# Performance work log

Hardware: AMD Instinct MI355X
Metric: run time of the kernel (lower is better)

Reference implementation:

```python
import jax, jax.numpy as jnp
import numpy as np

SLIDING_WINDOW = 512
LOGIT_SOFTCAP = 50.0
NEG_INF = -1e30


def setup_inputs() -> dict:
    key = jax.random.key(0)
    ks = jax.random.split(key, 3)
    B, S, H, KVH, D, BS = 4, 1024, 32, 8, 128, 64
    nb = S // BS          # blocks per sequence = 16
    nblocks = B * nb      # total cache blocks = 64
    total = B * S         # flattened tokens = 4096
    return {
        "query": jax.random.normal(ks[0], (total, H, D), dtype=jnp.float32),
        "key": jax.random.normal(ks[1], (total, KVH, D), dtype=jnp.float32),
        "value": jax.random.normal(ks[2], (total, KVH, D), dtype=jnp.float32),
        "k_cache": jnp.zeros((nblocks, BS, KVH, D), dtype=jnp.float32),
        "v_cache": jnp.zeros((nblocks, BS, KVH, D), dtype=jnp.float32),
        "block_offsets": jnp.arange(nblocks, dtype=jnp.int32).reshape(B, nb),
    }


def reference(query, key, value, k_cache, v_cache, block_offsets):
    B, nb = block_offsets.shape
    nblocks, BS, KVH, D = k_cache.shape
    S = nb * BS
    H = query.shape[1]
    G = H // KVH  # GQA group size
    scale = D ** -0.5

    flat_blocks = block_offsets.reshape(-1)  # [B*nb]
    # 1) write new keys/values into the paged cache per the block table
    k_cache = k_cache.at[flat_blocks].set(key.reshape(-1, BS, KVH, D))
    v_cache = v_cache.at[flat_blocks].set(value.reshape(-1, BS, KVH, D))
    # 2) gather per-sequence contiguous K/V from cache blocks
    k = k_cache[flat_blocks].reshape(B, S, KVH, D)
    v = v_cache[flat_blocks].reshape(B, S, KVH, D)

    q = query.reshape(B, S, KVH, G, D)
    scores = jnp.einsum("bqhgd,bkhd->bhgqk", q, k) * scale
    # logit softcapping (Gemma-style)
    scores = jnp.tanh(scores / LOGIT_SOFTCAP) * LOGIT_SOFTCAP
    # causal + sliding-window mask
    i = jnp.arange(S)[:, None]
    j = jnp.arange(S)[None, :]
    mask = (j <= i) & ((i - j) < SLIDING_WINDOW)
    scores = jnp.where(mask, scores, NEG_INF)
    p = jax.nn.softmax(scores, axis=-1)
    out = jnp.einsum("bhgqk,bkhd->bqhgd", p, v)
    return out.reshape(B * S, H, D)
```

## Files before the change

### kernel.cpp

```cpp
#include <hip/hip_runtime.h>
#include <hip/hip_bf16.h>

typedef __bf16 bf16_t;
typedef bf16_t bf16x8 __attribute__((ext_vector_type(8)));
typedef bf16_t bf16x4 __attribute__((ext_vector_type(4)));
typedef bf16_t bf16x2 __attribute__((ext_vector_type(2)));
typedef float f32x4 __attribute__((ext_vector_type(4)));

#define B_   4
#define S_   1024
#define H_   32
#define KVH_ 8
#define D_   128
#define WIN_ 512
#define KVD_ (KVH_ * D_)
#define LOG2E_ 1.4426950408889634f
#define C1_ (2.0f * (0.08838834764831845f / 50.0f) * LOG2E_)
#define K2_ (50.0f * LOG2E_)
#define NK22_ (-2.0f * K2_)
#define EXP2F_(x) __builtin_amdgcn_exp2f(x)

__global__ __launch_bounds__(512, 4) void attn_fwd(
    const float* __restrict__ Q, const float* __restrict__ K,
    const float* __restrict__ V, float* __restrict__ Out)
{
  const int fid = blockIdx.x + 32 * (blockIdx.y + 8 * (int)blockIdx.z);
  const int swz = (fid & 7) * 128 + (fid >> 3);
  const int i0  = (swz & 31) * 32;
  const int kvh = (swz >> 5) & 7;
  const int b   = swz >> 8;

  const int tid  = threadIdx.x;
  const int w    = tid >> 6;
  const int lane = tid & 63;
  const int m16  = lane & 15;
  const int quad = lane >> 4;
  const int g    = w & 3;
  const int rb   = w >> 2;
  const int h    = kvh * 4 + g;
  const int iw   = i0 + rb * 16;
  const int i    = iw + m16;
  const int sw16 = (m16 >> 1) & 3;

  __shared__ __align__(16) bf16_t KsB[2][32 * 128];
  __shared__ __align__(16) bf16_t VtB[2][128 * 32];
  __shared__ __align__(16) bf16_t PsB[8 * 16 * 32];

  bf16x8 qf[4];
  {
    const float* qp = Q + ((size_t)(b * S_ + iw + m16) * H_ + h) * D_;
    #pragma unroll
    for (int s = 0; s < 4; ++s) {
      const int d0 = 32 * s + 8 * quad;
      float4 f0 = *(const float4*)(qp + d0);
      float4 f1 = *(const float4*)(qp + d0 + 4);
      bf16x8 t = { (bf16_t)f0.x, (bf16_t)f0.y, (bf16_t)f0.z, (bf16_t)f0.w,
                   (bf16_t)f1.x, (bf16_t)f1.y, (bf16_t)f1.z, (bf16_t)f1.w };
      qf[s] = t;
    }
  }

  f32x4 O[8];
  #pragma unroll
  for (int c = 0; c < 8; ++c) O[c] = (f32x4){0.f, 0.f, 0.f, 0.f};
  f32x4 lacc = (f32x4){0.f, 0.f, 0.f, 0.f};

  const bool isK = (tid < 256);
  const int krow = tid >> 3;
  const int kseg = tid & 7;
  const float* ksrc = K + ((size_t)(b * S_ + krow) * KVH_ + kvh) * D_ + kseg * 16;
  const int koff0 = krow * 128 + (((2 * kseg)     ^ (krow & 15)) << 3);
  const int koff1 = krow * 128 + (((2 * kseg + 1) ^ (krow & 15)) << 3);
  const int vt  = tid & 255;
  const int tv  = (vt >> 4) * 2;
  const int mpr = vt & 15;
  const float* vsrc = V + ((size_t)(b * S_ + tv) * KVH_ + kvh) * D_ + mpr * 8;
  const int vbase = mpr * 256 + (tv & 7);
  const int vch   = (tv >> 3) ^ ((mpr >> 1) & 3);

  const int t_lo = (i0 >= WIN_) ? ((i0 - (WIN_ - 1)) >> 5) : 0;
  const int t_hi = i0 >> 5;

  float4 r0, r1, r2, r3;
  auto loadStage = [&](int j0v) {
    if (isK) {
      const float* p = ksrc + (size_t)j0v * KVD_;
      r0 = *(const float4*)(p);      r1 = *(const float4*)(p + 4);
      r2 = *(const float4*)(p + 8);  r3 = *(const float4*)(p + 12);
    } else {
      const float* p = vsrc + (size_t)j0v * KVD_;
      r0 = *(const float4*)(p);            r1 = *(const float4*)(p + 4);
      r2 = *(const float4*)(p + KVD_);     r3 = *(const float4*)(p + KVD_ + 4);
    }
  };
  auto writeStage = [&](int bi) {
    if (isK) {
      bf16x8 lo = { (bf16_t)r0.x, (bf16_t)r0.y, (bf16_t)r0.z, (bf16_t)r0.w,
                    (bf16_t)r1.x, (bf16_t)r1.y, (bf16_t)r1.z, (bf16_t)r1.w };
      bf16x8 hi = { (bf16_t)r2.x, (bf16_t)r2.y, (bf16_t)r2.z, (bf16_t)r2.w,
                    (bf16_t)r3.x, (bf16_t)r3.y, (bf16_t)r3.z, (bf16_t)r3.w };
      *(bf16x8*)&KsB[bi][koff0] = lo;
      *(bf16x8*)&KsB[bi][koff1] = hi;
    } else {
      const float av[8] = { r0.x, r0.y, r0.z, r0.w, r1.x, r1.y, r1.z, r1.w };
      const float bv[8] = { r2.x, r2.y, r2.z, r2.w, r3.x, r3.y, r3.z, r3.w };
      #pragma unroll
      for (int e = 0; e < 8; ++e) {
        bf16x2 pr = { (bf16_t)av[e], (bf16_t)bv[e] };
        *(bf16x2*)&VtB[bi][vbase + e * 32 + ((vch ^ (e >> 1)) << 3)] = pr;
      }
    }
  };

  loadStage(t_lo * 32);
  writeStage(0);
  __syncthreads();
  int buf = 0;

  for (int tb = t_lo; tb <= t_hi; ++tb) {
    const int j0  = tb * 32;
    const bool pre = (tb < t_hi);
    if (pre) loadStage(j0 + 32);

    if (!(j0 > iw + 15 || j0 + 31 < iw - (WIN_ - 1))) {
      const bool full = (j0 + 31 <= iw) && (iw + 15 - j0 < WIN_);
      const int pw = w * (16 * 32);

      #pragma unroll
      for (int t4 = 0; t4 < 2; ++t4) {
        f32x4 acc = (f32x4){0.f, 0.f, 0.f, 0.f};
        const int row = 16 * t4 + m16;
        __builtin_amdgcn_s_setprio(1);
        #pragma unroll
        for (int s = 0; s < 4; ++s) {
          bf16x8 a = *(const bf16x8*)&KsB[buf][row * 128 + (((quad + 4 * s) ^ m16) << 3)];
          acc = __builtin_amdgcn_mfma_f32_16x16x32_bf16(a, qf[s], acc, 0, 0, 0);
        }
        __builtin_amdgcn_s_setprio(0);
        bf16x4 pk;
        #pragma unroll
        for (int r = 0; r < 4; ++r) {
          float ez = EXP2F_(acc[r] * C1_);
          float p  = EXP2F_(NK22_ * __builtin_amdgcn_rcpf(ez + 1.f));
          if (!full) {
            const int j = j0 + t4 * 16 + 4 * quad + r;
            p = ((j <= i) && (i - j < WIN_)) ? p : 0.f;
          }
          lacc[r] += p;
          pk[r] = (bf16_t)p;
        }
        const int ch = (2 * t4 + (quad >> 1)) ^ sw16;
        *(bf16x4*)&PsB[pw + m16 * 32 + ch * 8 + (quad & 1) * 4] = pk;
      }
      bf16x8 pa = *(const bf16x8*)&PsB[pw + m16 * 32 + ((quad ^ sw16) << 3)];

      __builtin_amdgcn_s_setprio(1);
      #pragma unroll
      for (int c = 0; c < 8; ++c) {
        const int vrow = 16 * c + m16;
        bf16x8 v = *(const bf16x8*)&VtB[buf][vrow * 32 + (((quad ^ sw16) ^ (c & 3)) << 3)];
        O[c] = __builtin_amdgcn_mfma_f32_16x16x32_bf16(pa, v, O[c], 0, 0, 0);
      }
      __builtin_amdgcn_s_setprio(0);
    }

    if (pre) writeStage(buf ^ 1);
    __syncthreads();
    buf ^= 1;
  }

  float l_run = lacc[0] + lacc[1] + lacc[2] + lacc[3];
  l_run += __shfl_xor(l_run, 16);
  l_run += __shfl_xor(l_run, 32);

  float* ob = Out + ((size_t)(b * S_ + iw) * H_ + h) * D_;
  #pragma unroll
  for (int r = 0; r < 4; ++r) {
    const int rr = 4 * quad + r;
    const float lr = __shfl(l_run, rr);
    const float linv = __builtin_amdgcn_rcpf(lr);
    float* po = ob + (size_t)rr * (H_ * D_);
    #pragma unroll
    for (int c = 0; c < 8; ++c) po[c * 16 + m16] = O[c][r] * linv;
  }
}

extern "C" void kernel_launch(void* const* d_in, const int* in_sizes, int n_in,
                              void* d_out, int out_size, void* d_ws, size_t ws_size,
                              hipStream_t stream) {
  const float* q = (const float*)d_in[0];
  const float* k = (const float*)d_in[1];
  const float* v = (const float*)d_in[2];
  float* out = (float*)d_out;
  attn_fwd<<<dim3(S_ / 32, KVH_, B_), 512, 0, stream>>>(q, k, v, out);
}
```

Measured before the change: 210.0 us.

## Halve block to 4 waves, each wave computing two 16-row query tiles

The block drops from 8 waves to 4. Each wave now owns one head and both 16-row query sub-tiles, so every K and V fragment read from LDS feeds two MFMAs, and fewer threads cover the same tile. K/V staging is spread over 128 threads per tensor with more loads each. The K write-back is moved between QK and PV and the V write-back after PV, to overlap LDS writes with compute. The risks are higher register pressure (two O accumulator sets, more staging registers), lower occupancy with launch bounds of 3, and loss of the per-wave skip of fully masked tiles.

```diff
diff --git a/kernel.cpp b/kernel.cpp
--- a/kernel.cpp
+++ b/kernel.cpp
@@ -20,7 +20,7 @@
 #define NK22_ (-2.0f * K2_)
 #define EXP2F_(x) __builtin_amdgcn_exp2f(x)
 
-__global__ __launch_bounds__(512, 4) void attn_fwd(
+__global__ __launch_bounds__(256, 3) void attn_fwd(
     const float* __restrict__ Q, const float* __restrict__ K,
     const float* __restrict__ V, float* __restrict__ Out)
 {
@@ -35,20 +35,17 @@
   const int lane = tid & 63;
   const int m16  = lane & 15;
   const int quad = lane >> 4;
-  const int g    = w & 3;
-  const int rb   = w >> 2;
-  const int h    = kvh * 4 + g;
-  const int iw   = i0 + rb * 16;
-  const int i    = iw + m16;
+  const int h    = kvh * 4 + w;
   const int sw16 = (m16 >> 1) & 3;
 
   __shared__ __align__(16) bf16_t KsB[2][32 * 128];
   __shared__ __align__(16) bf16_t VtB[2][128 * 32];
-  __shared__ __align__(16) bf16_t PsB[8 * 16 * 32];
-
-  bf16x8 qf[4];
-  {
-    const float* qp = Q + ((size_t)(b * S_ + iw + m16) * H_ + h) * D_;
+  __shared__ __align__(16) bf16_t PsB[4 * 32 * 32];
+
+  bf16x8 qf[2][4];
+  #pragma unroll
+  for (int qb = 0; qb < 2; ++qb) {
+    const float* qp = Q + ((size_t)(b * S_ + i0 + qb * 16 + m16) * H_ + h) * D_;
     #pragma unroll
     for (int s = 0; s < 4; ++s) {
       const int d0 = 32 * s + 8 * quad;
@@ -56,132 +53,157 @@
       float4 f1 = *(const float4*)(qp + d0 + 4);
       bf16x8 t = { (bf16_t)f0.x, (bf16_t)f0.y, (bf16_t)f0.z, (bf16_t)f0.w,
                    (bf16_t)f1.x, (bf16_t)f1.y, (bf16_t)f1.z, (bf16_t)f1.w };
-      qf[s] = t;
+      qf[qb][s] = t;
     }
   }
 
-  f32x4 O[8];
+  f32x4 O[2][8];
   #pragma unroll
-  for (int c = 0; c < 8; ++c) O[c] = (f32x4){0.f, 0.f, 0.f, 0.f};
-  f32x4 lacc = (f32x4){0.f, 0.f, 0.f, 0.f};
-
-  const bool isK = (tid < 256);
-  const int krow = tid >> 3;
-  const int kseg = tid & 7;
-  const float* ksrc = K + ((size_t)(b * S_ + krow) * KVH_ + kvh) * D_ + kseg * 16;
-  const int koff0 = krow * 128 + (((2 * kseg)     ^ (krow & 15)) << 3);
-  const int koff1 = krow * 128 + (((2 * kseg + 1) ^ (krow & 15)) << 3);
-  const int vt  = tid & 255;
-  const int tv  = (vt >> 4) * 2;
-  const int mpr = vt & 15;
-  const float* vsrc = V + ((size_t)(b * S_ + tv) * KVH_ + kvh) * D_ + mpr * 8;
-  const int vbase = mpr * 256 + (tv & 7);
-  const int vch   = (tv >> 3) ^ ((mpr >> 1) & 3);
+  for (int qb = 0; qb < 2; ++qb)
+    #pragma unroll
+    for (int c = 0; c < 8; ++c) O[qb][c] = (f32x4){0.f, 0.f, 0.f, 0.f};
+  f32x4 lacc[2] = { (f32x4){0.f,0.f,0.f,0.f}, (f32x4){0.f,0.f,0.f,0.f} };
+
+  const bool isK = (w < 2);
+  const int kt   = tid & 127;
+  const int krow = kt >> 2;
+  const int kc0  = (kt & 3) * 4;
+  const float* kbase = K + ((size_t)(b * S_ + krow) * KVH_ + kvh) * D_ + kc0 * 8;
+  const int vtt  = tid & 127;
+  const int tv   = (vtt >> 3) * 2;
+  const int mgrp = vtt & 7;
+  const int d0v  = mgrp * 16;
+  const float* vbase = V + ((size_t)(b * S_ + tv) * KVH_ + kvh) * D_ + d0v;
 
   const int t_lo = (i0 >= WIN_) ? ((i0 - (WIN_ - 1)) >> 5) : 0;
   const int t_hi = i0 >> 5;
 
-  float4 r0, r1, r2, r3;
-  auto loadStage = [&](int j0v) {
+  float4 sr[8];
+  auto stage_load = [&](int j0n) {
     if (isK) {
-      const float* p = ksrc + (size_t)j0v * KVD_;
-      r0 = *(const float4*)(p);      r1 = *(const float4*)(p + 4);
-      r2 = *(const float4*)(p + 8);  r3 = *(const float4*)(p + 12);
+      const float* p = kbase + (size_t)j0n * KVD_;
+      #pragma unroll
+      for (int c = 0; c < 8; ++c) sr[c] = *(const float4*)(p + c * 4);
     } else {
-      const float* p = vsrc + (size_t)j0v * KVD_;
-      r0 = *(const float4*)(p);            r1 = *(const float4*)(p + 4);
-      r2 = *(const float4*)(p + KVD_);     r3 = *(const float4*)(p + KVD_ + 4);
+      const float* p = vbase + (size_t)j0n * KVD_;
+      #pragma unroll
+      for (int c = 0; c < 4; ++c) sr[c]     = *(const float4*)(p + c * 4);
+      #pragma unroll
+      for (int c = 0; c < 4; ++c) sr[4 + c] = *(const float4*)(p + KVD_ + c * 4);
     }
   };
-  auto writeStage = [&](int bi) {
-    if (isK) {
-      bf16x8 lo = { (bf16_t)r0.x, (bf16_t)r0.y, (bf16_t)r0.z, (bf16_t)r0.w,
-                    (bf16_t)r1.x, (bf16_t)r1.y, (bf16_t)r1.z, (bf16_t)r1.w };
-      bf16x8 hi = { (bf16_t)r2.x, (bf16_t)r2.y, (bf16_t)r2.z, (bf16_t)r2.w,
-                    (bf16_t)r3.x, (bf16_t)r3.y, (bf16_t)r3.z, (bf16_t)r3.w };
-      *(bf16x8*)&KsB[bi][koff0] = lo;
-      *(bf16x8*)&KsB[bi][koff1] = hi;
-    } else {
-      const float av[8] = { r0.x, r0.y, r0.z, r0.w, r1.x, r1.y, r1.z, r1.w };
-      const float bv[8] = { r2.x, r2.y, r2.z, r2.w, r3.x, r3.y, r3.z, r3.w };
-      #pragma unroll
-      for (int e = 0; e < 8; ++e) {
-        bf16x2 pr = { (bf16_t)av[e], (bf16_t)bv[e] };
-        *(bf16x2*)&VtB[bi][vbase + e * 32 + ((vch ^ (e >> 1)) << 3)] = pr;
-      }
+  auto stage_write_K = [&](int bi) {
+    #pragma unroll
+    for (int cc = 0; cc < 4; ++cc) {
+      const int ch = kc0 + cc;
+      float4 a = sr[2 * cc], bq = sr[2 * cc + 1];
+      bf16x8 o = { (bf16_t)a.x, (bf16_t)a.y, (bf16_t)a.z, (bf16_t)a.w,
+                   (bf16_t)bq.x, (bf16_t)bq.y, (bf16_t)bq.z, (bf16_t)bq.w };
+      *(bf16x8*)&KsB[bi][krow * 128 + ((ch ^ (krow & 15)) << 3)] = o;
     }
   };
-
-  loadStage(t_lo * 32);
-  writeStage(0);
+  auto stage_write_V = [&](int bi) {
+    #pragma unroll
+    for (int e = 0; e < 16; ++e) {
+      const int d   = d0v + e;
+      const int mpr = d >> 3, e7 = d & 7;
+      const float va = ((const float*)&sr[e >> 2])[e & 3];
+      const float vb = ((const float*)&sr[4 + (e >> 2)])[e & 3];
+      bf16x2 pr = { (bf16_t)va, (bf16_t)vb };
+      const int addr = mpr * 256 + e7 * 32 +
+                       ((((tv >> 3) ^ ((mpr >> 1) & 3) ^ (e7 >> 1))) << 3) +
+                       (tv & 7);
+      *(bf16x2*)&VtB[bi][addr] = pr;
+    }
+  };
+
+  stage_load(t_lo * 32);
+  if (isK) stage_write_K(0); else stage_write_V(0);
   __syncthreads();
   int buf = 0;
+
+  const int pw = w * (32 * 32);
 
   for (int tb = t_lo; tb <= t_hi; ++tb) {
     const int j0  = tb * 32;
     const bool pre = (tb < t_hi);
-    if (pre) loadStage(j0 + 32);
-
-    if (!(j0 > iw + 15 || j0 + 31 < iw - (WIN_ - 1))) {
-      const bool full = (j0 + 31 <= iw) && (iw + 15 - j0 < WIN_);
-      const int pw = w * (16 * 32);
-
-      #pragma unroll
-      for (int t4 = 0; t4 < 2; ++t4) {
-        f32x4 acc = (f32x4){0.f, 0.f, 0.f, 0.f};
-        const int row = 16 * t4 + m16;
-        __builtin_amdgcn_s_setprio(1);
-        #pragma unroll
-        for (int s = 0; s < 4; ++s) {
-          bf16x8 a = *(const bf16x8*)&KsB[buf][row * 128 + (((quad + 4 * s) ^ m16) << 3)];
-          acc = __builtin_amdgcn_mfma_f32_16x16x32_bf16(a, qf[s], acc, 0, 0, 0);
-        }
-        __builtin_amdgcn_s_setprio(0);
+    if (pre) stage_load(j0 + 32);
+
+    f32x4 acc[2][2];
+    #pragma unroll
+    for (int kb = 0; kb < 2; ++kb)
+      #pragma unroll
+      for (int qb = 0; qb < 2; ++qb) acc[kb][qb] = (f32x4){0.f,0.f,0.f,0.f};
+    __builtin_amdgcn_s_setprio(1);
+    #pragma unroll
+    for (int kb = 0; kb < 2; ++kb) {
+      const int row = 16 * kb + m16;
+      #pragma unroll
+      for (int s = 0; s < 4; ++s) {
+        bf16x8 a = *(const bf16x8*)&KsB[buf][row * 128 + (((quad + 4 * s) ^ m16) << 3)];
+        acc[kb][0] = __builtin_amdgcn_mfma_f32_16x16x32_bf16(a, qf[0][s], acc[kb][0], 0, 0, 0);
+        acc[kb][1] = __builtin_amdgcn_mfma_f32_16x16x32_bf16(a, qf[1][s], acc[kb][1], 0, 0, 0);
+      }
+    }
+    __builtin_amdgcn_s_setprio(0);
+
+    #pragma unroll
+    for (int kb = 0; kb < 2; ++kb)
+      #pragma unroll
+      for (int qb = 0; qb < 2; ++qb) {
+        const int iwq = i0 + qb * 16;
+        const bool fullb = (j0 + 16 * kb + 15 <= iwq) &&
+                           (iwq + 15 - (j0 + 16 * kb) < WIN_);
         bf16x4 pk;
         #pragma unroll
         for (int r = 0; r < 4; ++r) {
-          float ez = EXP2F_(acc[r] * C1_);
+          float ez = EXP2F_(acc[kb][qb][r] * C1_);
           float p  = EXP2F_(NK22_ * __builtin_amdgcn_rcpf(ez + 1.f));
-          if (!full) {
-            const int j = j0 + t4 * 16 + 4 * quad + r;
+          if (!fullb) {
+            const int j = j0 + 16 * kb + 4 * quad + r;
+            const int i = iwq + m16;
             p = ((j <= i) && (i - j < WIN_)) ? p : 0.f;
           }
-          lacc[r] += p;
+          lacc[qb][r] += p;
           pk[r] = (bf16_t)p;
         }
-        const int ch = (2 * t4 + (quad >> 1)) ^ sw16;
-        *(bf16x4*)&PsB[pw + m16 * 32 + ch * 8 + (quad & 1) * 4] = pk;
+        const int ch = (2 * kb + (quad >> 1)) ^ sw16;
+        *(bf16x4*)&PsB[pw + (qb * 16 + m16) * 32 + ch * 8 + (quad & 1) * 4] = pk;
       }
-      bf16x8 pa = *(const bf16x8*)&PsB[pw + m16 * 32 + ((quad ^ sw16) << 3)];
-
-      __builtin_amdgcn_s_setprio(1);
-      #pragma unroll
-      for (int c = 0; c < 8; ++c) {
-        const int vrow = 16 * c + m16;
-        bf16x8 v = *(const bf16x8*)&VtB[buf][vrow * 32 + (((quad ^ sw16) ^ (c & 3)) << 3)];
-        O[c] = __builtin_amdgcn_mfma_f32_16x16x32_bf16(pa, v, O[c], 0, 0, 0);
-      }
-      __builtin_amdgcn_s_setprio(0);
-    }
-
-    if (pre) writeStage(buf ^ 1);
+
+    if (pre && isK) stage_write_K(buf ^ 1);
+
+    bf16x8 pa0 = *(const bf16x8*)&PsB[pw + (m16)      * 32 + ((quad ^ sw16) << 3)];
+    bf16x8 pa1 = *(const bf16x8*)&PsB[pw + (16 + m16) * 32 + ((quad ^ sw16) << 3)];
+    __builtin_amdgcn_s_setprio(1);
+    #pragma unroll
+    for (int c = 0; c < 8; ++c) {
+      const int vrow = 16 * c + m16;
+      bf16x8 v = *(const bf16x8*)&VtB[buf][vrow * 32 + (((quad ^ sw16) ^ (c & 3)) << 3)];
+      O[0][c] = __builtin_amdgcn_mfma_f32_16x16x32_bf16(pa0, v, O[0][c], 0, 0, 0);
+      O[1][c] = __builtin_amdgcn_mfma_f32_16x16x32_bf16(pa1, v, O[1][c], 0, 0, 0);
+    }
+    __builtin_amdgcn_s_setprio(0);
+
+    if (pre && !isK) stage_write_V(buf ^ 1);
     __syncthreads();
     buf ^= 1;
   }
 
-  float l_run = lacc[0] + lacc[1] + lacc[2] + lacc[3];
-  l_run += __shfl_xor(l_run, 16);
-  l_run += __shfl_xor(l_run, 32);
-
-  float* ob = Out + ((size_t)(b * S_ + iw) * H_ + h) * D_;
   #pragma unroll
-  for (int r = 0; r < 4; ++r) {
-    const int rr = 4 * quad + r;
-    const float lr = __shfl(l_run, rr);
-    const float linv = __builtin_amdgcn_rcpf(lr);
-    float* po = ob + (size_t)rr * (H_ * D_);
-    #pragma unroll
-    for (int c = 0; c < 8; ++c) po[c * 16 + m16] = O[c][r] * linv;
+  for (int qb = 0; qb < 2; ++qb) {
+    float l = lacc[qb][0] + lacc[qb][1] + lacc[qb][2] + lacc[qb][3];
+    l += __shfl_xor(l, 16);
+    l += __shfl_xor(l, 32);
+    #pragma unroll
+    for (int r = 0; r < 4; ++r) {
+      const int rr = 4 * quad + r;
+      const float lr = __shfl(l, rr);
+      const float linv = __builtin_amdgcn_rcpf(lr);
+      float* po = Out + ((size_t)(b * S_ + i0 + qb * 16 + rr) * H_ + h) * D_;
+      #pragma unroll
+      for (int c = 0; c < 8; ++c) po[c * 16 + m16] = O[qb][c][r] * linv;
+    }
   }
 }
 
@@ -192,5 +214,5 @@
   const float* k = (const float*)d_in[1];
   const float* v = (const float*)d_in[2];
   float* out = (float*)d_out;
-  attn_fwd<<<dim3(S_ / 32, KVH_, B_), 512, 0, stream>>>(q, k, v, out);
+  attn_fwd<<<dim3(S_ / 32, KVH_, B_), 256, 0, stream>>>(q, k, v, out);
 }
```

Result: slower. 346.7 us (+65.1%).
